# Performance work log

Measured on AMD Instinct MI355X. Metric: run time of the kernel, lower is better.

## Reference

```python
import jax, jax.numpy as jnp
import numpy as np

UNITS = 1024
D_Q = 1024
D_V = 1024


def setup_inputs() -> dict:
    key = jax.random.key(0)
    ks = jax.random.split(key, 8)
    B, S = 32, 2048
    query = jax.random.normal(ks[0], (B, D_Q), dtype=jnp.float32)
    values = jax.random.normal(ks[1], (B, S, D_V), dtype=jnp.float32)
    # Keras Dense params (glorot-ish scale for weights, zero bias init kept random-free)
    W1 = jax.random.normal(ks[2], (D_V, UNITS), dtype=jnp.float32) / np.sqrt(D_V)
    b1 = jnp.zeros((UNITS,), dtype=jnp.float32)
    W2 = jax.random.normal(ks[3], (D_Q, UNITS), dtype=jnp.float32) / np.sqrt(D_Q)
    b2 = jnp.zeros((UNITS,), dtype=jnp.float32)
    V = jax.random.normal(ks[4], (UNITS, 1), dtype=jnp.float32) / np.sqrt(UNITS)
    bV = jnp.zeros((1,), dtype=jnp.float32)
    return {"query": query, "values": values, "W1": W1, "b1": b1,
            "W2": W2, "b2": b2, "V": V, "bV": bV}


def reference(query, values, W1, b1, W2, b2, V, bV):
    # query: [B, d_q], values: [B, S, d_v]
    proj_v = jnp.einsum('bsd,du->bsu', values, W1) + b1        # [B, S, U]
    proj_q = (query @ W2 + b2)[:, None, :]                      # [B, 1, U]
    score = jnp.tanh(proj_v + proj_q) @ V + bV                  # [B, S, 1]
    attention_weights = jax.nn.softmax(score, axis=1)           # [B, S, 1]
    context_vector = jnp.sum(attention_weights * values, axis=1)  # [B, d_v]
    return (context_vector, attention_weights)
```

## Files before the change

### kernel.cpp

```cpp
#include <hip/hip_runtime.h>
#include <math.h>

#define B_  32
#define S_  2048
#define DV  1024
#define U_  1024

typedef __attribute__((ext_vector_type(8))) short bf16x8;
typedef __attribute__((ext_vector_type(4))) float f32x4;

__device__ inline unsigned short f2bf(float f) {
    unsigned int x = __float_as_uint(f);
    return (unsigned short)((x + 0x7fffu + ((x >> 16) & 1u)) >> 16);
}

__device__ inline float tanh_fast(float x) {
    float ax = fabsf(x);
    float e  = __expf(ax + ax);
    float t  = 1.0f - __fdividef(2.0f, e + 1.0f);
    return copysignf(t, x);
}

__device__ __forceinline__ void gload16(const void* g, void* l) {
    __builtin_amdgcn_global_load_lds(
        (const __attribute__((address_space(1))) void*)g,
        (__attribute__((address_space(3))) void*)l,
        16, 0, 0);
}

#define ASM_VMCNT(N) asm volatile("s_waitcnt vmcnt(" #N ")" ::: "memory")
#define ASM_LGKM0()  do { asm volatile("s_waitcnt lgkmcnt(0)" ::: "memory"); \
                          __builtin_amdgcn_sched_barrier(0); } while (0)

__global__ void init_kernel(const float* __restrict__ b1, const float* __restrict__ b2,
                            float* __restrict__ t, float* __restrict__ ctx,
                            float* __restrict__ scores) {
    int i = blockIdx.x * 256 + threadIdx.x;
    scores[i] = 0.f;
    if (i < B_ * U_) {
        int u = i & (U_ - 1);
        t[i]   = b1[u] + b2[u];
        ctx[i] = 0.f;
    }
}

__global__ void projq_kernel(const float* __restrict__ q, const float* __restrict__ W2,
                             float* __restrict__ t) {
    int b  = blockIdx.x;
    int ks = blockIdx.y;
    int tid = threadIdx.x;
    __shared__ float qs[64];
    if (tid < 64) qs[tid] = q[b * DV + ks * 64 + tid];
    __syncthreads();
    float a0 = 0.f, a1 = 0.f, a2 = 0.f, a3 = 0.f;
    const float* w = W2 + (size_t)(ks * 64) * U_;
    for (int d = 0; d < 64; ++d) {
        float qd = qs[d];
        const float* wr = w + (size_t)d * U_ + tid;
        a0 += qd * wr[0];
        a1 += qd * wr[256];
        a2 += qd * wr[512];
        a3 += qd * wr[768];
    }
    atomicAdd(&t[b * U_ + tid      ], a0);
    atomicAdd(&t[b * U_ + tid + 256], a1);
    atomicAdd(&t[b * U_ + tid + 512], a2);
    atomicAdd(&t[b * U_ + tid + 768], a3);
}

__global__ void cvt_values(const float* __restrict__ v, unsigned short* __restrict__ o) {
    size_t i = ((size_t)blockIdx.x * 256 + threadIdx.x) * 8;
    float4 f0 = *(const float4*)(v + i);
    float4 f1 = *(const float4*)(v + i + 4);
    union { unsigned short s[8]; uint4 u; } p;
    p.s[0] = f2bf(f0.x); p.s[1] = f2bf(f0.y); p.s[2] = f2bf(f0.z); p.s[3] = f2bf(f0.w);
    p.s[4] = f2bf(f1.x); p.s[5] = f2bf(f1.y); p.s[6] = f2bf(f1.z); p.s[7] = f2bf(f1.w);
    *(uint4*)(o + i) = p.u;
}

__global__ void prep_w1t(const float* __restrict__ W1, unsigned short* __restrict__ W1T) {
    __shared__ float tile[64][65];
    int k0 = blockIdx.x * 64, u0 = blockIdx.y * 64;
    int t = threadIdx.x;
    int lr = t >> 4, lc = (t & 15) * 4;
#pragma unroll
    for (int i = 0; i < 4; ++i) {
        float4 f = *(const float4*)&W1[(size_t)(k0 + lr + i * 16) * U_ + u0 + lc];
        tile[lr + i * 16][lc + 0] = f.x; tile[lr + i * 16][lc + 1] = f.y;
        tile[lr + i * 16][lc + 2] = f.z; tile[lr + i * 16][lc + 3] = f.w;
    }
    __syncthreads();
    int ur = t >> 2, kq = (t & 3) * 16;
    union { unsigned short s[8]; uint4 u; } p0, p1;
#pragma unroll
    for (int e = 0; e < 8; ++e) p0.s[e] = f2bf(tile[kq + e][ur]);
#pragma unroll
    for (int e = 0; e < 8; ++e) p1.s[e] = f2bf(tile[kq + 8 + e][ur]);
    unsigned short* dst = W1T + (size_t)(u0 + ur) * 1024 + k0 + kq;
    *(uint4*)dst       = p0.u;
    *(uint4*)(dst + 8) = p1.u;
}

#define MFMA16(MB, NB)                                                          \
    _Pragma("unroll") for (int ks = 0; ks < 2; ++ks)                            \
    _Pragma("unroll") for (int n = 0; n < 2; ++n)                               \
    _Pragma("unroll") for (int m = 0; m < 4; ++m)                               \
        acc[(MB)+m][(NB)+n] = __builtin_amdgcn_mfma_f32_16x16x32_bf16(          \
            af[m][ks], bf[n][ks], acc[(MB)+m][(NB)+n], 0, 0, 0);

__launch_bounds__(512, 2)
__global__ void scores_mfma8(const unsigned short* __restrict__ Abf,
                             const unsigned short* __restrict__ W1T,
                             const float* __restrict__ tvec,
                             const float* __restrict__ V,
                             float* __restrict__ scores) {
    __shared__ __align__(16) char lds[131072];

    const int tid  = threadIdx.x;
    const int lane = tid & 63;
    const int wave = tid >> 6;
    const int wm   = wave >> 2;
    const int wn   = wave & 3;
    const int l15  = lane & 15;
    const int lq   = lane >> 4;

    const int id    = blockIdx.x;
    const int wg    = (id & 7) * 128 + (id >> 3);
    const int utile = wg & 3;
    const int stile = wg >> 2;
    const size_t row0 = (size_t)stile * 256;
    const int b       = (int)(row0 >> 11);
    const int s_local = (int)(row0 & 2047);
    const int u0      = utile * 256;

    const int rowst = wave * 8 + (lane >> 3);
    const int kch8  = ((lane & 7) ^ ((lane >> 3) & 7)) * 8;
    const unsigned short* aSrc = Abf + (row0 + rowst) * 1024 + kch8;
    const unsigned short* bSrc = W1T + (size_t)(u0 + rowst) * 1024 + kch8;
    char* const dstW = lds + wave * 1024;

    const int ao0 = wm * 16384 + l15 * 128 + ((lq ^ (l15 & 7)) << 4);
    const int ao1 = ao0 ^ 64;
    const int bo0 = 32768 + (wn >> 1) * 16384 + (wn & 1) * 8192
                  + l15 * 128 + ((lq ^ (l15 & 7)) << 4);
    const int bo1 = bo0 ^ 64;

    f32x4 acc[8][4];
#pragma unroll
    for (int m = 0; m < 8; ++m)
#pragma unroll
        for (int n = 0; n < 4; ++n) acc[m][n] = (f32x4)0.f;

    bf16x8 af[4][2];
    bf16x8 bf[2][2];

    auto stage2 = [&](const unsigned short* s, int dOff) {
        gload16(s,             dstW + dOff);
        gload16(s + 64 * 1024, dstW + dOff + 8192);
    };
    auto readA4 = [&](int base) {
#pragma unroll
        for (int m = 0; m < 4; ++m) {
            af[m][0] = *(const bf16x8*)(lds + base + m * 2048 + ao0);
            af[m][1] = *(const bf16x8*)(lds + base + m * 2048 + ao1);
        }
    };
    auto readB2 = [&](int base) {
#pragma unroll
        for (int n = 0; n < 2; ++n) {
            bf[n][0] = *(const bf16x8*)(lds + base + n * 2048 + bo0);
            bf[n][1] = *(const bf16x8*)(lds + base + n * 2048 + bo1);
        }
    };

    stage2(aSrc,          0);
    stage2(aSrc + 131072, 16384);
    stage2(bSrc,          32768);
    stage2(bSrc + 131072, 49152);
    stage2(aSrc + 64,     65536);
    __builtin_amdgcn_sched_barrier(0);
    ASM_VMCNT(2);
    __builtin_amdgcn_s_barrier();
    __builtin_amdgcn_sched_barrier(0);

    for (int it = 0; it < 8; ++it) {
        const bool pf = (it < 7);
        readA4(0);
        readB2(0);
        stage2(aSrc + 64 + 131072, 81920);
        __builtin_amdgcn_s_barrier();
        ASM_LGKM0();
        __builtin_amdgcn_s_setprio(1);
        MFMA16(0, 0);
        __builtin_amdgcn_s_setprio(0);
        __builtin_amdgcn_s_barrier();
        readB2(2 * 2048);
        stage2(bSrc + 64, 98304);
        __builtin_amdgcn_s_barrier();
        ASM_LGKM0();
        __builtin_amdgcn_s_setprio(1);
        MFMA16(0, 2);
        __builtin_amdgcn_s_setprio(0);
        __builtin_amdgcn_s_barrier();
        readA4(4 * 2048);
        stage2(bSrc + 64 + 131072, 114688);
        __builtin_amdgcn_s_barrier();
        ASM_LGKM0();
        __builtin_amdgcn_s_setprio(1);
        MFMA16(4, 2);
        __builtin_amdgcn_s_setprio(0);
        __builtin_amdgcn_s_barrier();
        readB2(0);
        if (pf) stage2(aSrc + 128, 0);
        __builtin_amdgcn_s_barrier();
        ASM_LGKM0();
        __builtin_amdgcn_s_setprio(1);
        MFMA16(4, 0);
        __builtin_amdgcn_s_setprio(0);
        __builtin_amdgcn_sched_barrier(0);
        if (pf) { ASM_VMCNT(2); } else { ASM_VMCNT(0); }
        __builtin_amdgcn_s_barrier();
        __builtin_amdgcn_sched_barrier(0);
        readA4(65536);
        readB2(65536);
        if (pf) stage2(aSrc + 128 + 131072, 16384);
        __builtin_amdgcn_s_barrier();
        ASM_LGKM0();
        __builtin_amdgcn_s_setprio(1);
        MFMA16(0, 0);
        __builtin_amdgcn_s_setprio(0);
        __builtin_amdgcn_s_barrier();
        readB2(65536 + 2 * 2048);
        if (pf) stage2(bSrc + 128, 32768);
        __builtin_amdgcn_s_barrier();
        ASM_LGKM0();
        __builtin_amdgcn_s_setprio(1);
        MFMA16(0, 2);
        __builtin_amdgcn_s_setprio(0);
        __builtin_amdgcn_s_barrier();
        readA4(65536 + 4 * 2048);
        if (pf) stage2(bSrc + 128 + 131072, 49152);
        __builtin_amdgcn_s_barrier();
        ASM_LGKM0();
        __builtin_amdgcn_s_setprio(1);
        MFMA16(4, 2);
        __builtin_amdgcn_s_setprio(0);
        __builtin_amdgcn_s_barrier();
        readB2(65536);
        if (pf) stage2(aSrc + 192, 65536);
        __builtin_amdgcn_s_barrier();
        ASM_LGKM0();
        __builtin_amdgcn_s_setprio(1);
        MFMA16(4, 0);
        __builtin_amdgcn_s_setprio(0);
        __builtin_amdgcn_sched_barrier(0);
        if (pf) { ASM_VMCNT(2); }
        __builtin_amdgcn_s_barrier();
        __builtin_amdgcn_sched_barrier(0);

        aSrc += 128;
        bSrc += 128;
    }

    __syncthreads();
    float* fscore = (float*)lds;
    if (tid < 256) fscore[tid] = 0.f;
    __syncthreads();
    float tu[4], vu[4];
#pragma unroll
    for (int n = 0; n < 4; ++n) {
        int u = u0 + wn * 64 + n * 16 + l15;
        tu[n] = tvec[b * U_ + u];
        vu[n] = V[u];
    }
#pragma unroll
    for (int m = 0; m < 8; ++m) {
#pragma unroll
        for (int r = 0; r < 4; ++r) {
            float p = 0.f;
#pragma unroll
            for (int n = 0; n < 4; ++n) p += tanh_fast(acc[m][n][r] + tu[n]) * vu[n];
            p += __shfl_xor(p, 1);
            p += __shfl_xor(p, 2);
            p += __shfl_xor(p, 4);
            p += __shfl_xor(p, 8);
            if (l15 == 0) atomicAdd(&fscore[wm * 128 + m * 16 + lq * 4 + r], p);
        }
    }
    __syncthreads();
    if (tid < 256) atomicAdd(&scores[(size_t)b * S_ + s_local + tid], fscore[tid]);
}

template<bool ABF16>
__launch_bounds__(256, 2)
__global__ void scores_mfma(const void* __restrict__ aPtr,
                            const unsigned short* __restrict__ W1T,
                            const float* __restrict__ t,
                            const float* __restrict__ V,
                            float* __restrict__ scores) {
    __shared__ unsigned short sA[128 * 40];
    __shared__ unsigned short sB[256 * 40];
    __shared__ float fscore[128];

    const int tid  = threadIdx.x;
    const int lane = tid & 63;
    const int wave = tid >> 6;
    const int wm = wave & 1, wn = wave >> 1;
    const int l15 = lane & 15, lq = lane >> 4;

    const int id    = blockIdx.x;
    const int utile = (id >> 3) & 3;
    const int stile = (id & 7) | ((id >> 5) << 3);
    const size_t row0 = (size_t)stile * 128;
    const int b       = (int)(row0 >> 11);
    const int s_local = (int)(row0 & 2047);
    const int u0      = utile * 256;

    if (tid < 128) fscore[tid] = 0.f;

    const int ar = tid >> 1, ak = (tid & 1) << 4;
    const int br = tid >> 1, bk = (tid & 1) << 4;

    const float* Af = (const float*)aPtr + (row0 + ar) * 1024 + ak;
    const unsigned short* Ab = (const unsigned short*)aPtr + (row0 + ar) * 1024 + ak;
    const unsigned short* Bp0 = W1T + (size_t)(u0 + br) * 1024 + bk;
    const unsigned short* Bp1 = Bp0 + 128 * 1024;

    f32x4 acc[4][8];
#pragma unroll
    for (int i = 0; i < 4; ++i)
#pragma unroll
        for (int j = 0; j < 8; ++j) acc[i][j] = (f32x4)0.f;

    uint4 sa0, sa1, sb0, sb1, sb2, sb3;
    float4 fa0, fa1, fa2, fa3;

    if (ABF16) {
        sa0 = *(const uint4*)(Ab);
        sa1 = *(const uint4*)(Ab + 8);
    } else {
        fa0 = *(const float4*)(Af);
        fa1 = *(const float4*)(Af + 4);
        fa2 = *(const float4*)(Af + 8);
        fa3 = *(const float4*)(Af + 12);
    }
    sb0 = *(const uint4*)(Bp0);
    sb1 = *(const uint4*)(Bp0 + 8);
    sb2 = *(const uint4*)(Bp1);
    sb3 = *(const uint4*)(Bp1 + 8);

    for (int k0 = 0; k0 < 1024; k0 += 32) {
        __syncthreads();
        if (ABF16) {
            *(uint4*)&sA[ar * 40 + ak]     = sa0;
            *(uint4*)&sA[ar * 40 + ak + 8] = sa1;
        } else {
            union { unsigned short s[8]; uint4 u; } p0, p1;
            p0.s[0] = f2bf(fa0.x); p0.s[1] = f2bf(fa0.y); p0.s[2] = f2bf(fa0.z); p0.s[3] = f2bf(fa0.w);
            p0.s[4] = f2bf(fa1.x); p0.s[5] = f2bf(fa1.y); p0.s[6] = f2bf(fa1.z); p0.s[7] = f2bf(fa1.w);
            p1.s[0] = f2bf(fa2.x); p1.s[1] = f2bf(fa2.y); p1.s[2] = f2bf(fa2.z); p1.s[3] = f2bf(fa2.w);
            p1.s[4] = f2bf(fa3.x); p1.s[5] = f2bf(fa3.y); p1.s[6] = f2bf(fa3.z); p1.s[7] = f2bf(fa3.w);
            *(uint4*)&sA[ar * 40 + ak]     = p0.u;
            *(uint4*)&sA[ar * 40 + ak + 8] = p1.u;
        }
        *(uint4*)&sB[br * 40 + bk]           = sb0;
        *(uint4*)&sB[br * 40 + bk + 8]       = sb1;
        *(uint4*)&sB[(br + 128) * 40 + bk]     = sb2;
        *(uint4*)&sB[(br + 128) * 40 + bk + 8] = sb3;

        if (k0 + 32 < 1024) {
            int nk = k0 + 32;
            if (ABF16) {
                sa0 = *(const uint4*)(Ab + nk);
                sa1 = *(const uint4*)(Ab + nk + 8);
            } else {
                fa0 = *(const float4*)(Af + nk);
                fa1 = *(const float4*)(Af + nk + 4);
                fa2 = *(const float4*)(Af + nk + 8);
                fa3 = *(const float4*)(Af + nk + 12);
            }
            sb0 = *(const uint4*)(Bp0 + nk);
            sb1 = *(const uint4*)(Bp0 + nk + 8);
            sb2 = *(const uint4*)(Bp1 + nk);
            sb3 = *(const uint4*)(Bp1 + nk + 8);
        }
        __syncthreads();

        bf16x8 af[4];
#pragma unroll
        for (int i = 0; i < 4; ++i)
            af[i] = *(const bf16x8*)&sA[(64 * wm + 16 * i + l15) * 40 + lq * 8];
#pragma unroll
        for (int j = 0; j < 8; ++j) {
            bf16x8 bfj = *(const bf16x8*)&sB[(128 * wn + 16 * j + l15) * 40 + lq * 8];
#pragma unroll
            for (int i = 0; i < 4; ++i)
                acc[i][j] = __builtin_amdgcn_mfma_f32_16x16x32_bf16(af[i], bfj, acc[i][j], 0, 0, 0);
        }
    }

    float tu[8], vu[8];
#pragma unroll
    for (int j = 0; j < 8; ++j) {
        int u = u0 + 128 * wn + 16 * j + l15;
        tu[j] = t[b * U_ + u];
        vu[j] = V[u];
    }
#pragma unroll
    for (int i = 0; i < 4; ++i) {
#pragma unroll
        for (int r = 0; r < 4; ++r) {
            float p = 0.f;
#pragma unroll
            for (int j = 0; j < 8; ++j) p += tanh_fast(acc[i][j][r] + tu[j]) * vu[j];
            p += __shfl_xor(p, 1);
            p += __shfl_xor(p, 2);
            p += __shfl_xor(p, 4);
            p += __shfl_xor(p, 8);
            if (l15 == 0) atomicAdd(&fscore[64 * wm + 16 * i + lq * 4 + r], p);
        }
    }
    __syncthreads();
    if (tid < 128) atomicAdd(&scores[(size_t)b * S_ + s_local + tid], fscore[tid]);
}

__launch_bounds__(256, 2)
__global__ void scores_vec(const float* __restrict__ values, const float* __restrict__ W1,
                           const float* __restrict__ t, const float* __restrict__ V,
                           float* __restrict__ scores) {
    __shared__ float vA[16][132];
    __shared__ float vB[16][68];
    __shared__ float fscore[128];
    const int b   = blockIdx.y;
    const int s0  = blockIdx.x * 128;
    const int tid = threadIdx.x;
    const int tx  = tid & 15, ty = tid >> 4;
    if (tid < 128) fscore[tid] = 0.f;
    const float* vbase = values + ((size_t)b * S_ + s0) * (size_t)DV;
    const int lm = tid >> 2, lkq = (tid & 3) * 4;
    const int lbk = tid >> 4, lbj = (tid & 15) * 4;
    for (int nt = 0; nt < U_ / 64; ++nt) {
        const int u0 = nt * 64;
        float acc[8][4];
#pragma unroll
        for (int i = 0; i < 8; ++i)
#pragma unroll
            for (int j = 0; j < 4; ++j) acc[i][j] = 0.f;
        for (int k0 = 0; k0 < DV; k0 += 16) {
            __syncthreads();
            const float4 v0 = *(const float4*)(vbase + (size_t)lm * DV + k0 + lkq);
            const float4 v1 = *(const float4*)(vbase + (size_t)(lm + 64) * DV + k0 + lkq);
            vA[lkq + 0][lm] = v0.x; vA[lkq + 1][lm] = v0.y;
            vA[lkq + 2][lm] = v0.z; vA[lkq + 3][lm] = v0.w;
            vA[lkq + 0][lm + 64] = v1.x; vA[lkq + 1][lm + 64] = v1.y;
            vA[lkq + 2][lm + 64] = v1.z; vA[lkq + 3][lm + 64] = v1.w;
            *(float4*)&vB[lbk][lbj] = *(const float4*)(W1 + (size_t)(k0 + lbk) * U_ + u0 + lbj);
            __syncthreads();
#pragma unroll
            for (int k = 0; k < 16; ++k) {
                float4 va0 = *(const float4*)&vA[k][ty * 8];
                float4 va1 = *(const float4*)&vA[k][ty * 8 + 4];
                float4 vb  = *(const float4*)&vB[k][tx * 4];
                float a_[8] = {va0.x, va0.y, va0.z, va0.w, va1.x, va1.y, va1.z, va1.w};
                float b_[4] = {vb.x, vb.y, vb.z, vb.w};
#pragma unroll
                for (int i = 0; i < 8; ++i)
#pragma unroll
                    for (int j = 0; j < 4; ++j) acc[i][j] += a_[i] * b_[j];
            }
        }
        float tq[4], vv[4];
#pragma unroll
        for (int j = 0; j < 4; ++j) {
            int u = u0 + tx * 4 + j;
            tq[j] = t[b * U_ + u];
            vv[j] = V[u];
        }
#pragma unroll
        for (int i = 0; i < 8; ++i) {
            float p = 0.f;
#pragma unroll
            for (int j = 0; j < 4; ++j) p += tanhf(acc[i][j] + tq[j]) * vv[j];
            p += __shfl_down(p, 8, 16);
            p += __shfl_down(p, 4, 16);
            p += __shfl_down(p, 2, 16);
            p += __shfl_down(p, 1, 16);
            if (tx == 0) fscore[ty * 8 + i] += p;
        }
    }
    __syncthreads();
    if (tid < 128) scores[(size_t)b * S_ + s0 + tid] = fscore[tid];
}

__global__ void softmax_kernel(const float* __restrict__ scores, float* __restrict__ wout) {
    int b = blockIdx.x;
    int tid = threadIdx.x;
    __shared__ float red[256];
    float v[8];
    float m = -1e30f;
#pragma unroll
    for (int i = 0; i < 8; ++i) {
        v[i] = scores[(size_t)b * S_ + tid + i * 256];
        m = fmaxf(m, v[i]);
    }
    red[tid] = m; __syncthreads();
    for (int off = 128; off > 0; off >>= 1) {
        if (tid < off) red[tid] = fmaxf(red[tid], red[tid + off]);
        __syncthreads();
    }
    m = red[0];
    __syncthreads();
    float s = 0.f;
#pragma unroll
    for (int i = 0; i < 8; ++i) { v[i] = __expf(v[i] - m); s += v[i]; }
    red[tid] = s; __syncthreads();
    for (int off = 128; off > 0; off >>= 1) {
        if (tid < off) red[tid] += red[tid + off];
        __syncthreads();
    }
    float inv = 1.f / red[0];
#pragma unroll
    for (int i = 0; i < 8; ++i) wout[(size_t)b * S_ + tid + i * 256] = v[i] * inv;
}

__global__ void context_kernel(const float* __restrict__ values, const float* __restrict__ w,
                               float* __restrict__ ctx) {
    int b  = blockIdx.x;
    int dc = blockIdx.y;
    int sc = blockIdx.z;
    int tid = threadIdx.x;
    int d = dc * 256 + tid;
    __shared__ float ws_[256];
    ws_[tid] = w[(size_t)b * S_ + sc * 256 + tid];
    __syncthreads();
    float acc = 0.f;
    const float* vp = values + ((size_t)b * S_ + sc * 256) * (size_t)DV + d;
#pragma unroll 4
    for (int s = 0; s < 256; ++s) acc += ws_[s] * vp[(size_t)s * DV];
    atomicAdd(&ctx[b * DV + d], acc);
}

extern "C" void kernel_launch(void* const* d_in, const int* in_sizes, int n_in,
                              void* d_out, int out_size, void* d_ws, size_t ws_size,
                              hipStream_t stream) {
    const float* query  = (const float*)d_in[0];
    const float* values = (const float*)d_in[1];
    const float* W1     = (const float*)d_in[2];
    const float* b1     = (const float*)d_in[3];
    const float* W2     = (const float*)d_in[4];
    const float* b2     = (const float*)d_in[5];
    const float* V      = (const float*)d_in[6];

    float* out  = (float*)d_out;
    float* ctx  = out;
    float* wout = out + B_ * DV;

    char* ws = (char*)d_ws;
    const size_t W1T_BYTES = (size_t)U_ * DV * 2;
    const size_t T_BYTES   = (size_t)B_ * U_ * 4;
    const size_t SC_BYTES  = (size_t)B_ * S_ * 4;
    const size_t ABF_BYTES = (size_t)B_ * S_ * DV * 2;

    if (ws_size >= W1T_BYTES + T_BYTES + SC_BYTES + ABF_BYTES) {
        unsigned short* W1T = (unsigned short*)ws;
        float* t      = (float*)(ws + W1T_BYTES);
        float* scores = t + B_ * U_;
        unsigned short* Abf = (unsigned short*)(scores + B_ * S_);

        init_kernel   <<<dim3(256),      256, 0, stream>>>(b1, b2, t, ctx, scores);
        projq_kernel  <<<dim3(32, 16),   256, 0, stream>>>(query, W2, t);
        cvt_values    <<<dim3(32768),    256, 0, stream>>>(values, Abf);
        prep_w1t      <<<dim3(16, 16),   256, 0, stream>>>(W1, W1T);
        scores_mfma8  <<<dim3(1024),     512, 0, stream>>>(Abf, W1T, t, V, scores);
        softmax_kernel<<<dim3(32),       256, 0, stream>>>(scores, wout);
        context_kernel<<<dim3(32, 4, 8), 256, 0, stream>>>(values, wout, ctx);
    } else if (ws_size >= W1T_BYTES + T_BYTES + SC_BYTES) {
        unsigned short* W1T = (unsigned short*)ws;
        float* t      = (float*)(ws + W1T_BYTES);
        float* scores = t + B_ * U_;

        init_kernel   <<<dim3(256),      256, 0, stream>>>(b1, b2, t, ctx, scores);
        projq_kernel  <<<dim3(32, 16),   256, 0, stream>>>(query, W2, t);
        prep_w1t      <<<dim3(16, 16),   256, 0, stream>>>(W1, W1T);
        scores_mfma<false><<<dim3(2048), 256, 0, stream>>>(values, W1T, t, V, scores);
        softmax_kernel<<<dim3(32),       256, 0, stream>>>(scores, wout);
        context_kernel<<<dim3(32, 4, 8), 256, 0, stream>>>(values, wout, ctx);
    } else {
        float* t      = (float*)ws;
        float* scores = t + B_ * U_;

        init_kernel   <<<dim3(256),      256, 0, stream>>>(b1, b2, t, ctx, scores);
        projq_kernel  <<<dim3(32, 16),   256, 0, stream>>>(query, W2, t);
        scores_vec    <<<dim3(16, 32),   256, 0, stream>>>(values, W1, t, V, scores);
        softmax_kernel<<<dim3(32),       256, 0, stream>>>(scores, wout);
        context_kernel<<<dim3(32, 4, 8), 256, 0, stream>>>(values, wout, ctx);
    }
}
```

Measured before the change: 597.8 us.

## Pre-tile bf16 values into swizzled LDS layout and vectorize context kernel

The fp32-to-bf16 conversion kernel now writes values in a pre-tiled, pre-swizzled block layout that matches the LDS image the MFMA scores kernel expects. Each wave's A-tile global loads then become contiguous 1KB chunks instead of strided row segments. The context kernel is also changed to use float4 loads over all 1024 dims per block, with 128-row sequence chunks. The scattered writes in the conversion kernel may cost some write efficiency.

Result: no change. 603.9 us (+1.0%).

```diff
diff --git a/kernel.cpp b/kernel.cpp
--- a/kernel.cpp
+++ b/kernel.cpp
@@ -68,14 +68,22 @@
     atomicAdd(&t[b * U_ + tid + 768], a3);
 }
 
-__global__ void cvt_values(const float* __restrict__ v, unsigned short* __restrict__ o) {
-    size_t i = ((size_t)blockIdx.x * 256 + threadIdx.x) * 8;
+__global__ void cvt_values_tiled(const float* __restrict__ v, char* __restrict__ o) {
+    size_t t = (size_t)blockIdx.x * 256 + threadIdx.x;
+    size_t i = t * 8;
+    int row = (int)(i >> 10);
+    int k   = (int)(i & 1023);
     float4 f0 = *(const float4*)(v + i);
     float4 f1 = *(const float4*)(v + i + 4);
     union { unsigned short s[8]; uint4 u; } p;
     p.s[0] = f2bf(f0.x); p.s[1] = f2bf(f0.y); p.s[2] = f2bf(f0.z); p.s[3] = f2bf(f0.w);
     p.s[4] = f2bf(f1.x); p.s[5] = f2bf(f1.y); p.s[6] = f2bf(f1.z); p.s[7] = f2bf(f1.w);
-    *(uint4*)(o + i) = p.u;
+    int stile = row >> 8, rt = row & 255, h = rt >> 7, r = rt & 127;
+    int kt = k >> 6, kk = k & 63;
+    int pchunk = (kk >> 3) ^ (r & 7);
+    size_t dst = (size_t)stile * 524288 + (size_t)kt * 32768
+               + h * 16384 + r * 128 + pchunk * 16;
+    *(uint4*)(o + dst) = p.u;
 }
 
 __global__ void prep_w1t(const float* __restrict__ W1, unsigned short* __restrict__ W1T) {
@@ -109,7 +117,7 @@
             af[m][ks], bf[n][ks], acc[(MB)+m][(NB)+n], 0, 0, 0);
 
 __launch_bounds__(512, 2)
-__global__ void scores_mfma8(const unsigned short* __restrict__ Abf,
+__global__ void scores_mfma8(const char* __restrict__ AbfT,
                              const unsigned short* __restrict__ W1T,
                              const float* __restrict__ tvec,
                              const float* __restrict__ V,
@@ -133,9 +141,9 @@
     const int s_local = (int)(row0 & 2047);
     const int u0      = utile * 256;
 
+    const char* aBase = AbfT + (size_t)stile * 524288 + wave * 1024 + lane * 16;
     const int rowst = wave * 8 + (lane >> 3);
     const int kch8  = ((lane & 7) ^ ((lane >> 3) & 7)) * 8;
-    const unsigned short* aSrc = Abf + (row0 + rowst) * 1024 + kch8;
     const unsigned short* bSrc = W1T + (size_t)(u0 + rowst) * 1024 + kch8;
     char* const dstW = lds + wave * 1024;
 
@@ -154,7 +162,11 @@
     bf16x8 af[4][2];
     bf16x8 bf[2][2];
 
-    auto stage2 = [&](const unsigned short* s, int dOff) {
+    auto stageA = [&](size_t gOff, int dOff) {
+        gload16(aBase + gOff,        dstW + dOff);
+        gload16(aBase + gOff + 8192, dstW + dOff + 8192);
+    };
+    auto stageB = [&](const unsigned short* s, int dOff) {
         gload16(s,             dstW + dOff);
         gload16(s + 64 * 1024, dstW + dOff + 8192);
     };
@@ -173,11 +185,11 @@
         }
     };
 
-    stage2(aSrc,          0);
-    stage2(aSrc + 131072, 16384);
-    stage2(bSrc,          32768);
-    stage2(bSrc + 131072, 49152);
-    stage2(aSrc + 64,     65536);
+    stageA(0,     0);
+    stageA(16384, 16384);
+    stageB(bSrc,          32768);
+    stageB(bSrc + 131072, 49152);
+    stageA(32768, 65536);
     __builtin_amdgcn_sched_barrier(0);
     ASM_VMCNT(2);
     __builtin_amdgcn_s_barrier();
@@ -185,9 +197,10 @@
 
     for (int it = 0; it < 8; ++it) {
         const bool pf = (it < 7);
+        const size_t aIt = (size_t)it * 65536;
         readA4(0);
         readB2(0);
-        stage2(aSrc + 64 + 131072, 81920);
+        stageA(aIt + 49152, 81920);
         __builtin_amdgcn_s_barrier();
         ASM_LGKM0();
         __builtin_amdgcn_s_setprio(1);
@@ -195,7 +208,7 @@
         __builtin_amdgcn_s_setprio(0);
         __builtin_amdgcn_s_barrier();
         readB2(2 * 2048);
-        stage2(bSrc + 64, 98304);
+        stageB(bSrc + 64, 98304);
         __builtin_amdgcn_s_barrier();
         ASM_LGKM0();
         __builtin_amdgcn_s_setprio(1);
@@ -203,7 +216,7 @@
         __builtin_amdgcn_s_setprio(0);
         __builtin_amdgcn_s_barrier();
         readA4(4 * 2048);
-        stage2(bSrc + 64 + 131072, 114688);
+        stageB(bSrc + 64 + 131072, 114688);
         __builtin_amdgcn_s_barrier();
         ASM_LGKM0();
         __builtin_amdgcn_s_setprio(1);
@@ -211,7 +224,7 @@
         __builtin_amdgcn_s_setprio(0);
         __builtin_amdgcn_s_barrier();
         readB2(0);
-        if (pf) stage2(aSrc + 128, 0);
+        if (pf) stageA(aIt + 65536, 0);
         __builtin_amdgcn_s_barrier();
         ASM_LGKM0();
         __builtin_amdgcn_s_setprio(1);
@@ -223,7 +236,7 @@
         __builtin_amdgcn_sched_barrier(0);
         readA4(65536);
         readB2(65536);
-        if (pf) stage2(aSrc + 128 + 131072, 16384);
+        if (pf) stageA(aIt + 81920, 16384);
         __builtin_amdgcn_s_barrier();
         ASM_LGKM0();
         __builtin_amdgcn_s_setprio(1);
@@ -231,7 +244,7 @@
         __builtin_amdgcn_s_setprio(0);
         __builtin_amdgcn_s_barrier();
         readB2(65536 + 2 * 2048);
-        if (pf) stage2(bSrc + 128, 32768);
+        if (pf) stageB(bSrc + 128, 32768);
         __builtin_amdgcn_s_barrier();
         ASM_LGKM0();
         __builtin_amdgcn_s_setprio(1);
@@ -239,7 +252,7 @@
         __builtin_amdgcn_s_setprio(0);
         __builtin_amdgcn_s_barrier();
         readA4(65536 + 4 * 2048);
-        if (pf) stage2(bSrc + 128 + 131072, 49152);
+        if (pf) stageB(bSrc + 128 + 131072, 49152);
         __builtin_amdgcn_s_barrier();
         ASM_LGKM0();
         __builtin_amdgcn_s_setprio(1);
@@ -247,7 +260,7 @@
         __builtin_amdgcn_s_setprio(0);
         __builtin_amdgcn_s_barrier();
         readB2(65536);
-        if (pf) stage2(aSrc + 192, 65536);
+        if (pf) stageA(aIt + 98304, 65536);
         __builtin_amdgcn_s_barrier();
         ASM_LGKM0();
         __builtin_amdgcn_s_setprio(1);
@@ -258,7 +271,6 @@
         __builtin_amdgcn_s_barrier();
         __builtin_amdgcn_sched_barrier(0);
 
-        aSrc += 128;
         bSrc += 128;
     }
 
@@ -525,19 +537,23 @@
 
 __global__ void context_kernel(const float* __restrict__ values, const float* __restrict__ w,
                                float* __restrict__ ctx) {
-    int b  = blockIdx.x;
-    int dc = blockIdx.y;
-    int sc = blockIdx.z;
+    int b   = blockIdx.x;
+    int sc  = blockIdx.y;
     int tid = threadIdx.x;
-    int d = dc * 256 + tid;
-    __shared__ float ws_[256];
-    ws_[tid] = w[(size_t)b * S_ + sc * 256 + tid];
-    __syncthreads();
-    float acc = 0.f;
-    const float* vp = values + ((size_t)b * S_ + sc * 256) * (size_t)DV + d;
+    __shared__ float ws_[128];
+    if (tid < 128) ws_[tid] = w[(size_t)b * S_ + sc * 128 + tid];
+    __syncthreads();
+    const float4* vp = (const float4*)(values + ((size_t)b * S_ + sc * 128) * DV) + tid;
+    float ax = 0.f, ay = 0.f, az = 0.f, aw = 0.f;
 #pragma unroll 4
-    for (int s = 0; s < 256; ++s) acc += ws_[s] * vp[(size_t)s * DV];
-    atomicAdd(&ctx[b * DV + d], acc);
+    for (int s = 0; s < 128; ++s) {
+        float4 v = vp[(size_t)s * 256];
+        float wv = ws_[s];
+        ax += wv * v.x; ay += wv * v.y; az += wv * v.z; aw += wv * v.w;
+    }
+    float* c = ctx + b * DV + tid * 4;
+    atomicAdd(c + 0, ax); atomicAdd(c + 1, ay);
+    atomicAdd(c + 2, az); atomicAdd(c + 3, aw);
 }
 
 extern "C" void kernel_launch(void* const* d_in, const int* in_sizes, int n_in,
@@ -565,15 +581,15 @@
         unsigned short* W1T = (unsigned short*)ws;
         float* t      = (float*)(ws + W1T_BYTES);
         float* scores = t + B_ * U_;
-        unsigned short* Abf = (unsigned short*)(scores + B_ * S_);
-
-        init_kernel   <<<dim3(256),      256, 0, stream>>>(b1, b2, t, ctx, scores);
-        projq_kernel  <<<dim3(32, 16),   256, 0, stream>>>(query, W2, t);
-        cvt_values    <<<dim3(32768),    256, 0, stream>>>(values, Abf);
-        prep_w1t      <<<dim3(16, 16),   256, 0, stream>>>(W1, W1T);
-        scores_mfma8  <<<dim3(1024),     512, 0, stream>>>(Abf, W1T, t, V, scores);
-        softmax_kernel<<<dim3(32),       256, 0, stream>>>(scores, wout);
-        context_kernel<<<dim3(32, 4, 8), 256, 0, stream>>>(values, wout, ctx);
+        char*  AbfT   = (char*)(scores + B_ * S_);
+
+        init_kernel     <<<dim3(256),      256, 0, stream>>>(b1, b2, t, ctx, scores);
+        projq_kernel    <<<dim3(32, 16),   256, 0, stream>>>(query, W2, t);
+        cvt_values_tiled<<<dim3(32768),    256, 0, stream>>>(values, AbfT);
+        prep_w1t        <<<dim3(16, 16),   256, 0, stream>>>(W1, W1T);
+        scores_mfma8    <<<dim3(1024),     512, 0, stream>>>(AbfT, W1T, t, V, scores);
+        softmax_kernel  <<<dim3(32),       256, 0, stream>>>(scores, wout);
+        context_kernel  <<<dim3(32, 16),   256, 0, stream>>>(values, wout, ctx);
     } else if (ws_size >= W1T_BYTES + T_BYTES + SC_BYTES) {
         unsigned short* W1T = (unsigned short*)ws;
         float* t      = (float*)(ws + W1T_BYTES);
@@ -584,7 +600,7 @@
         prep_w1t      <<<dim3(16, 16),   256, 0, stream>>>(W1, W1T);
         scores_mfma<false><<<dim3(2048), 256, 0, stream>>>(values, W1T, t, V, scores);
         softmax_kernel<<<dim3(32),       256, 0, stream>>>(scores, wout);
-        context_kernel<<<dim3(32, 4, 8), 256, 0, stream>>>(values, wout, ctx);
+        context_kernel<<<dim3(32, 16),   256, 0, stream>>>(values, wout, ctx);
     } else {
         float* t      = (float*)ws;
         float* scores = t + B_ * U_;
@@ -593,6 +609,6 @@
         projq_kernel  <<<dim3(32, 16),   256, 0, stream>>>(query, W2, t);
         scores_vec    <<<dim3(16, 32),   256, 0, stream>>>(values, W1, t, V, scores);
         softmax_kernel<<<dim3(32),       256, 0, stream>>>(scores, wout);
-        context_kernel<<<dim3(32, 4, 8), 256, 0, stream>>>(values, wout, ctx);
-    }
-}
+        context_kernel<<<dim3(32, 16),   256, 0, stream>>>(values, wout, ctx);
+    }
+}
```
